# Kernel tuning notes

Measured on AMD Instinct MI355X. Metric: run time of the kernel, lower is better.

Reference implementation:

```python
import jax, jax.numpy as jnp
import numpy as np

HEADS = 8  # from init_kwargs

def setup_inputs() -> dict:
    key = jax.random.key(0)
    ks = jax.random.split(key, 9)
    N, S, E = 8, 2048, 512
    scale = 1.0 / np.sqrt(E)
    return {
        "values": jax.random.normal(ks[0], (N, S, E), jnp.float32),
        "keys": jax.random.normal(ks[1], (N, S, E), jnp.float32),
        "query": jax.random.normal(ks[2], (N, S, E), jnp.float32),
        "mask": jnp.ones((N, 1, 1, S), jnp.int32),
        "Wv": jax.random.normal(ks[3], (E, E), jnp.float32) * scale,
        "Wk": jax.random.normal(ks[4], (E, E), jnp.float32) * scale,
        "Wq": jax.random.normal(ks[5], (E, E), jnp.float32) * scale,
        "Wo": jax.random.normal(ks[6], (E, E), jnp.float32) * scale,
        "bo": jnp.zeros((E,), jnp.float32),
    }

def reference(values, keys, query, mask, Wv, Wk, Wq, Wo, bo):
    N, Q, E = query.shape
    H = HEADS
    D = E // H
    v = (values @ Wv).reshape(N, -1, H, D)  # [N,K,H,D]
    k = (keys @ Wk).reshape(N, -1, H, D)
    q = (query @ Wq).reshape(N, Q, H, D)
    energy = jnp.einsum('nqhd,nkhd->nhqk', q, k)  # [N,H,Q,K]
    energy = jnp.where(mask == 0, jnp.float32(-1e20), energy)
    attn = jax.nn.softmax(energy / jnp.sqrt(jnp.float32(D)), axis=3)
    out = jnp.einsum('nhqk,nkhd->nqhd', attn, v).reshape(N, Q, E)
    return out @ Wo + bo
```

## Files before the change

kernel.cpp:

```cpp
#include <hip/hip_runtime.h>
#include <hip/hip_bf16.h>
#include <stdint.h>

typedef __bf16 bf16;
typedef __bf16 bf16x8 __attribute__((ext_vector_type(8)));
typedef __bf16 bf16x4v __attribute__((ext_vector_type(4)));
typedef float  f32x4  __attribute__((ext_vector_type(4)));
typedef float  f32x16 __attribute__((ext_vector_type(16)));
typedef unsigned int u32x4 __attribute__((ext_vector_type(4)));

#define NB    8
#define SEQ   2048
#define EMB   512
#define NHEAD 8
#define HD    64

static __device__ __forceinline__ f32x4 mfma16(bf16x8 a, bf16x8 b, f32x4 c) {
    return __builtin_amdgcn_mfma_f32_16x16x32_bf16(a, b, c, 0, 0, 0);
}
static __device__ __forceinline__ f32x16 mfma32(bf16x8 a, bf16x8 b, f32x16 c) {
    return __builtin_amdgcn_mfma_f32_32x32x16_bf16(a, b, c, 0, 0, 0);
}
static __device__ __forceinline__ float ex2(float x) {
    float r; asm("v_exp_f32 %0, %1" : "=v"(r) : "v"(x)); return r;
}
static __device__ __forceinline__ unsigned pkbf(float lo, float hi) {
    unsigned d; asm("v_cvt_pk_bf16_f32 %0, %1, %2" : "=v"(d) : "v"(lo), "v"(hi)); return d;
}
static __device__ __forceinline__ void gload_lds16(const void* g, void* l) {
    __builtin_amdgcn_global_load_lds(
        (const __attribute__((address_space(1))) unsigned int*)g,
        (__attribute__((address_space(3))) unsigned int*)l, 16, 0, 0);
}
static __device__ __forceinline__ int vposInv(int pos) {
    int p4  = pos >> 4;
    int r   = ((p4 & 1) << 3) | (pos & 7);
    int hi2 = (pos >> 3) & 1;
    return (p4 >> 1) * 32 + ((r & 3) | (hi2 << 2) | ((r >> 2) << 3));
}
#define PRIO1 __builtin_amdgcn_s_setprio(1)
#define PRIO0 __builtin_amdgcn_s_setprio(0)

__global__ __launch_bounds__(256) void prep_weights(
    const float* __restrict__ Wv, const float* __restrict__ Wk,
    const float* __restrict__ Wq, const float* __restrict__ Wo,
    bf16* __restrict__ wt)
{
    __shared__ float Ls[64][65];
    const int b    = blockIdx.x;
    const int wsel = b >> 6;
    const int kt   = (b & 63) >> 3;
    const int nt   = b & 7;
    const int t    = threadIdx.x;
    const float* src = (wsel == 0) ? Wv : (wsel == 1) ? Wk : (wsel == 2) ? Wq : Wo;

#pragma unroll
    for (int i = 0; i < 16; ++i) {
        int e = i * 256 + t;
        int k = e >> 6, n = e & 63;
        Ls[k][n] = src[(size_t)(kt * 64 + k) * 512 + nt * 64 + n];
    }
    __syncthreads();
#pragma unroll
    for (int i = 0; i < 16; ++i) {
        int e = i * 256 + t;
        int n = e >> 6, k = e & 63;
        wt[(size_t)wsel * 262144 + (size_t)(nt * 64 + n) * 512 + kt * 64 + k] = (bf16)Ls[k][n];
    }
}

__global__ __launch_bounds__(256) void proj_fused(
    const float* __restrict__ Av, const float* __restrict__ Ak,
    const float* __restrict__ Aq, const bf16* __restrict__ wt,
    bf16* __restrict__ VbP, bf16* __restrict__ Kb, bf16* __restrict__ Qb,
    float sc)
{
    __shared__ __align__(16) char smem[35328];
    bf16* As = (bf16*)smem;
    char* BsB = smem + 18432;

    const int t    = threadIdx.x;
    const int lane = t & 63;
    const int wave = t >> 6;
    const int wr   = wave >> 1, wc = wave & 1;
    const int l15  = lane & 15, lg = lane >> 4;
    const int z    = blockIdx.z;
    const long row0 = (long)blockIdx.x * 128;
    const int  col0 = blockIdx.y * 128;

    const float* A  = (z == 0) ? Av : (z == 1) ? Ak : Aq;
    const bf16*  Bt = wt + (size_t)z * 262144;
    const float  oscale = (z == 2) ? sc : 1.0f;

    f32x4 acc[4][4];
#pragma unroll
    for (int i = 0; i < 4; i++)
#pragma unroll
        for (int j = 0; j < 4; j++) acc[i][j] = (f32x4){0.f, 0.f, 0.f, 0.f};

    for (int k0 = 0; k0 < 512; k0 += 64) {
        __syncthreads();
#pragma unroll
        for (int i = 0; i < 8; i++) {
            int c  = t + 256 * i;
            int r  = c >> 4;
            int cc = (c & 15) * 4;
            f32x4 v = *(const f32x4*)(A + (row0 + r) * 512 + k0 + cc);
            bf16x4v pk = { (bf16)v[0], (bf16)v[1], (bf16)v[2], (bf16)v[3] };
            *(bf16x4v*)(As + r * 72 + cc) = pk;
        }
#pragma unroll
        for (int i = 0; i < 4; i++) {
            int chunk = i * 4 + wave;
            int c = chunk * 64 + lane;
            int r = c >> 3, u = c & 7;
            gload_lds16(Bt + (size_t)(col0 + r) * 512 + k0 + ((u ^ (r & 7)) << 3),
                        BsB + chunk * 1024);
        }
        __syncthreads();
#pragma unroll
        for (int kc = 0; kc < 64; kc += 32) {
            bf16x8 af[4], bfv[4];
#pragma unroll
            for (int mb = 0; mb < 4; mb++)
                af[mb] = *(bf16x8*)(As + (wr * 64 + mb * 16 + l15) * 72 + kc + lg * 8);
#pragma unroll
            for (int nb = 0; nb < 4; nb++) {
                int row = wc * 64 + nb * 16 + l15;
                bfv[nb] = *(bf16x8*)(BsB + row * 128 + (((lg + (kc >> 3)) ^ (l15 & 7)) << 4));
            }
#pragma unroll
            for (int mb = 0; mb < 4; mb++)
#pragma unroll
                for (int nb = 0; nb < 4; nb++)
                    acc[mb][nb] = mfma16(af[mb], bfv[nb], acc[mb][nb]);
        }
    }

    if (z == 0) {
        __syncthreads();
        bf16* Cs = (bf16*)smem;
#pragma unroll
        for (int mb = 0; mb < 4; mb++)
#pragma unroll
            for (int nb = 0; nb < 4; nb++)
#pragma unroll
                for (int r = 0; r < 4; r++) {
                    int keyl = wr * 64 + mb * 16 + lg * 4 + r;
                    int dl   = wc * 64 + nb * 16 + l15;
                    Cs[dl * 138 + keyl] = (bf16)acc[mb][nb][r];
                }
        __syncthreads();
        const int n_idx = (int)(row0 >> 11);
        const int key0  = (int)(row0 & 2047);
        const int dl    = t >> 1;
        const int half  = t & 1;
        const int x8    = (dl & 7) << 3;
        bf16* dst = VbP + ((size_t)n_idx * 512 + col0 + dl) * 2048 + key0 + half * 64;
#pragma unroll
        for (int cc = 0; cc < 8; ++cc) {
            bf16x8 v;
#pragma unroll
            for (int j = 0; j < 8; ++j)
                v[j] = Cs[dl * 138 + half * 64 + vposInv((cc * 8 + j) ^ x8)];
            *(bf16x8*)(dst + cc * 8) = v;
        }
    } else {
        bf16* Cp = (z == 1) ? Kb : Qb;
#pragma unroll
        for (int mb = 0; mb < 4; mb++)
#pragma unroll
            for (int nb = 0; nb < 4; nb++)
#pragma unroll
                for (int r = 0; r < 4; r++) {
                    long grow = row0 + wr * 64 + mb * 16 + lg * 4 + r;
                    int  gcol = col0 + wc * 64 + nb * 16 + l15;
                    Cp[grow * 512 + gcol] = (bf16)(acc[mb][nb][r] * oscale);
                }
    }
}

__global__ __launch_bounds__(256) void gemm_final(
    const bf16* __restrict__ Ap, const bf16* __restrict__ Bt,
    float* __restrict__ Cp, const float* __restrict__ bias)
{
    __shared__ __align__(16) char AsM[128 * 128];
    __shared__ __align__(16) bf16 Bs[128][64];

    const int t    = threadIdx.x;
    const int lane = t & 63;
    const int wave = t >> 6;
    const int wr   = wave >> 1, wc = wave & 1;
    const int l15  = lane & 15, lg = lane >> 4;
    const long row0 = (long)blockIdx.x * 128;
    const int  col0 = blockIdx.y * 128;

    f32x4 acc[4][4];
#pragma unroll
    for (int i = 0; i < 4; i++)
#pragma unroll
        for (int j = 0; j < 4; j++) acc[i][j] = (f32x4){0.f, 0.f, 0.f, 0.f};

    for (int k0 = 0; k0 < 512; k0 += 64) {
        __syncthreads();
#pragma unroll
        for (int i = 0; i < 4; i++) {
            int chunk = i * 4 + wave;
            int c = chunk * 64 + lane;
            int r = c >> 3, u = c & 7;
            gload_lds16(Ap + (row0 + r) * 512 + k0 + ((u ^ (r & 7)) << 3),
                        AsM + chunk * 1024);
        }
#pragma unroll
        for (int i = 0; i < 4; i++) {
            int chunk = i * 4 + wave;
            int c = chunk * 64 + lane;
            int r = c >> 3, u = c & 7;
            gload_lds16(Bt + (size_t)(col0 + r) * 512 + k0 + ((u ^ (r & 7)) << 3),
                        (char*)&Bs[0][0] + chunk * 1024);
        }
        __syncthreads();
#pragma unroll
        for (int kc = 0; kc < 64; kc += 32) {
            bf16x8 af[4], bfv[4];
#pragma unroll
            for (int mb = 0; mb < 4; mb++) {
                int row = wr * 64 + mb * 16 + l15;
                af[mb] = *(bf16x8*)(AsM + row * 128 + (((lg + (kc >> 3)) ^ (l15 & 7)) << 4));
            }
#pragma unroll
            for (int nb = 0; nb < 4; nb++) {
                int row = wc * 64 + nb * 16 + l15;
                bfv[nb] = *(bf16x8*)((char*)&Bs[0][0] + row * 128 + (((lg + (kc >> 3)) ^ (l15 & 7)) << 4));
            }
#pragma unroll
            for (int mb = 0; mb < 4; mb++)
#pragma unroll
                for (int nb = 0; nb < 4; nb++)
                    acc[mb][nb] = mfma16(af[mb], bfv[nb], acc[mb][nb]);
        }
    }

#pragma unroll
    for (int mb = 0; mb < 4; mb++)
#pragma unroll
        for (int nb = 0; nb < 4; nb++)
#pragma unroll
            for (int r = 0; r < 4; r++) {
                long grow = row0 + wr * 64 + mb * 16 + lg * 4 + r;
                int  gcol = col0 + wc * 64 + nb * 16 + l15;
                Cp[grow * 512 + gcol] = acc[mb][nb][r] + bias[gcol];
            }
}

__global__ __launch_bounds__(512, 2) void attn_kernel(
    const bf16* __restrict__ Qg, const bf16* __restrict__ Kg,
    const bf16* __restrict__ VbP, const int* __restrict__ mask,
    bf16* __restrict__ ctx)
{
    __shared__ __align__(16) char smem[65536];

    const int t    = threadIdx.x;
    const int lane = t & 63;
    const int w    = t >> 6;
    const int l31  = lane & 31;
    const int hi   = lane >> 5;
    const int h = blockIdx.x, n = blockIdx.y, qt = blockIdx.z;

    const size_t nbase   = (size_t)n * SEQ;
    const size_t headoff = (size_t)h * 64;
    const int q0 = qt * 256 + w * 32;

    {
        const int* mp0 = mask + n * SEQ + t * 4;
        int mok = (mp0[0] != 0) & (mp0[1] != 0) & (mp0[2] != 0) & (mp0[3] != 0);
        unsigned long long b = __ballot(mok);
        if (lane == 0) ((int*)smem)[w] = (b == ~0ULL) ? 1 : 0;
    }
    __syncthreads();
    int maskall = 1;
#pragma unroll
    for (int i = 0; i < 8; ++i) maskall &= ((int*)smem)[i];
    __syncthreads();

    bf16x8 qf[4];
#pragma unroll
    for (int ds = 0; ds < 4; ++ds)
        qf[ds] = *(const bf16x8*)(Qg + (nbase + q0 + l31) * 512 + headoff + ds * 16 + hi * 8);

    f32x16 o[2] = {};
    float l_run = 0.f;

    const bf16* kg = Kg + (nbase + w * 8 + (lane >> 3)) * 512 + headoff + (((lane & 7) ^ (lane >> 3)) << 3);
    const bf16* vgP = VbP + ((size_t)n * 512 + h * 64 + w * 8 + (lane >> 3)) * 2048 + ((lane & 7) << 3);
    const int*  mp = mask + n * SEQ;

    gload_lds16(kg,                    smem + 0 * 8192 + w * 1024);
    gload_lds16(kg + (size_t)64 * 512, smem + 1 * 8192 + w * 1024);
    gload_lds16(vgP,                   smem + 32768 + 0 * 8192 + w * 1024);
    gload_lds16(vgP + 64,              smem + 32768 + 1 * 8192 + w * 1024);
    __syncthreads();

    f32x16 p[2];
    u32x4  bq[4];

#define QK_TILE(BUF) do {                                                     \
        const char* kbb = smem + (BUF) * 8192;                                \
        f32x16 zz = {};                                                       \
        p[0] = zz; p[1] = zz;                                                 \
        PRIO1;                                                                \
        _Pragma("unroll")                                                     \
        for (int ds = 0; ds < 4; ++ds) {                                      \
            int sw = (ds * 32 + hi * 16) ^ ((l31 & 7) << 4);                  \
            bf16x8 kf0 = *(const bf16x8*)(kbb + l31 * 128 + sw);              \
            bf16x8 kf1 = *(const bf16x8*)(kbb + (32 + l31) * 128 + sw);       \
            p[0] = mfma32(kf0, qf[ds], p[0]);                                 \
            p[1] = mfma32(kf1, qf[ds], p[1]);                                 \
        }                                                                     \
        PRIO0;                                                                \
    } while (0)

#define MASK_TILE(T) do {                                                     \
        if (!maskall) {                                                       \
            int mv = mp[(T) * 64 + lane];                                     \
            unsigned long long mb = __ballot(mv != 0);                        \
            if (mb != ~0ULL) {                                                \
                _Pragma("unroll") for (int kb = 0; kb < 2; ++kb) {            \
                    float* pp = (float*)&p[kb];                               \
                    _Pragma("unroll") for (int r = 0; r < 16; ++r) {          \
                        int kk = kb * 32 + (r & 3) + 8 * (r >> 2) + 4 * hi;   \
                        if (!((mb >> kk) & 1)) pp[r] = -1e30f;                \
                    }                                                         \
                }                                                             \
            }                                                                 \
        }                                                                     \
    } while (0)

#define SM_PACK do {                                                          \
        float* p0 = (float*)&p[0];                                            \
        float* p1 = (float*)&p[1];                                            \
        float sa0 = 0.f, sa1 = 0.f, sa2 = 0.f, sa3 = 0.f;                     \
        _Pragma("unroll") for (int r = 0; r < 16; r += 4) {                   \
            float e0 = ex2(p0[r]);   p0[r]   = e0; sa0 += e0;                 \
            float e1 = ex2(p0[r+1]); p0[r+1] = e1; sa1 += e1;                 \
            float e2 = ex2(p0[r+2]); p0[r+2] = e2; sa2 += e2;                 \
            float e3 = ex2(p0[r+3]); p0[r+3] = e3; sa3 += e3;                 \
        }                                                                     \
        _Pragma("unroll") for (int r = 0; r < 16; r += 4) {                   \
            float e0 = ex2(p1[r]);   p1[r]   = e0; sa0 += e0;                 \
            float e1 = ex2(p1[r+1]); p1[r+1] = e1; sa1 += e1;                 \
            float e2 = ex2(p1[r+2]); p1[r+2] = e2; sa2 += e2;                 \
            float e3 = ex2(p1[r+3]); p1[r+3] = e3; sa3 += e3;                 \
        }                                                                     \
        float sl = (sa0 + sa1) + (sa2 + sa3);                                 \
        l_run += sl + __shfl_xor(sl, 32);                                     \
        _Pragma("unroll")                                                     \
        for (int ks = 0; ks < 4; ++ks) {                                      \
            float* ps = (ks >> 1) ? p1 : p0;                                  \
            int bo = (ks & 1) * 8;                                            \
            bq[ks] = (u32x4){ pkbf(ps[bo + 0], ps[bo + 1]),                   \
                              pkbf(ps[bo + 2], ps[bo + 3]),                   \
                              pkbf(ps[bo + 4], ps[bo + 5]),                   \
                              pkbf(ps[bo + 6], ps[bo + 7]) };                 \
        }                                                                     \
    } while (0)

#define PV_TILE(BUF) do {                                                     \
        const char* vbb = smem + 32768 + (BUF) * 8192;                        \
        PRIO1;                                                                \
        _Pragma("unroll")                                                     \
        for (int ks = 0; ks < 4; ++ks) {                                      \
            int sw = (ks * 32 + hi * 16) ^ ((l31 & 7) << 4);                  \
            bf16x8 vf0 = *(const bf16x8*)(vbb + l31 * 128 + sw);              \
            bf16x8 vf1 = *(const bf16x8*)(vbb + (32 + l31) * 128 + sw);       \
            union { u32x4 u; bf16x8 v; } c0;                                  \
            c0.u = bq[ks];                                                    \
            o[0] = mfma32(vf0, c0.v, o[0]);                                   \
            o[1] = mfma32(vf1, c0.v, o[1]);                                   \
        }                                                                     \
        PRIO0;                                                                \
    } while (0)

    for (int e = 0; e < 16; ++e) {
        const int bA = (e & 1) * 2, bB = bA + 1;
        const int nA = bA ^ 2,      nB = bB ^ 2;
        if (e < 15) {
            gload_lds16(kg + (size_t)(2 * e + 2) * 64 * 512, smem + nA * 8192 + w * 1024);
            gload_lds16(kg + (size_t)(2 * e + 3) * 64 * 512, smem + nB * 8192 + w * 1024);
            gload_lds16(vgP + (2 * e + 2) * 64, smem + 32768 + nA * 8192 + w * 1024);
            gload_lds16(vgP + (2 * e + 3) * 64, smem + 32768 + nB * 8192 + w * 1024);
        }
        QK_TILE(bA);
        MASK_TILE(2 * e);
        SM_PACK;
        PV_TILE(bA);
        QK_TILE(bB);
        MASK_TILE(2 * e + 1);
        SM_PACK;
        PV_TILE(bB);
        __syncthreads();
    }

    {
        float inv = 1.f / l_run;
        bf16* ob = (bf16*)(smem + w * 4608);
#pragma unroll
        for (int db = 0; db < 2; ++db) {
            float* oo = (float*)&o[db];
#pragma unroll
            for (int r = 0; r < 16; ++r) {
                int d = db * 32 + (r & 3) + 8 * (r >> 2) + 4 * hi;
                ob[l31 * 72 + d] = (bf16)(oo[r] * inv);
            }
        }
        __syncthreads();
#pragma unroll
        for (int i = 0; i < 2; ++i)
#pragma unroll
            for (int half = 0; half < 2; ++half) {
                int ql = i * 16 + (lane >> 2);
                int d8 = (lane & 3) * 8 + half * 32;
                bf16x8 vv = *(const bf16x8*)(ob + ql * 72 + d8);
                *(bf16x8*)(ctx + (nbase + q0 + ql) * 512 + headoff + d8) = vv;
            }
    }
#undef QK_TILE
#undef MASK_TILE
#undef SM_PACK
#undef PV_TILE
}

extern "C" void kernel_launch(void* const* d_in, const int* in_sizes, int n_in,
                              void* d_out, int out_size, void* d_ws, size_t ws_size,
                              hipStream_t stream) {
    (void)in_sizes; (void)n_in; (void)out_size; (void)ws_size;
    const float* values = (const float*)d_in[0];
    const float* keys   = (const float*)d_in[1];
    const float* query  = (const float*)d_in[2];
    const int*   mask   = (const int*)d_in[3];
    const float* Wv = (const float*)d_in[4];
    const float* Wk = (const float*)d_in[5];
    const float* Wq = (const float*)d_in[6];
    const float* Wo = (const float*)d_in[7];
    const float* bo = (const float*)d_in[8];
    float* out = (float*)d_out;

    char* ws = (char*)d_ws;
    bf16* wt  = (bf16*)(ws);
    bf16* Qb  = (bf16*)(ws + ((size_t)2  << 20));
    bf16* Kb  = (bf16*)(ws + ((size_t)18 << 20));
    bf16* VbP = (bf16*)(ws + ((size_t)34 << 20));
    bf16* Cb  = (bf16*)(ws + ((size_t)50 << 20));

    const float SC = 0.18033688011f;

    prep_weights<<<256, 256, 0, stream>>>(Wv, Wk, Wq, Wo, wt);
    proj_fused<<<dim3(128, 4, 3), 256, 0, stream>>>(values, keys, query, wt,
                                                    VbP, Kb, Qb, SC);
    attn_kernel<<<dim3(8, 8, 8), 512, 0, stream>>>(Qb, Kb, VbP, mask, Cb);
    gemm_final<<<dim3(128, 4), 256, 0, stream>>>(Cb, wt + 3 * 262144, out, bo);
}
```

Measured before the change: 154.2 us.

## Double-buffer LDS tiles in projection and output GEMMs to overlap loads

Both the fused QKV projection GEMM and the final output GEMM now use two LDS buffers per operand. The next K-slice is prefetched while MFMAs run on the current one, and one barrier per iteration replaces two. The aim is to hide global-load latency behind compute. In exchange, LDS use roughly doubles (about 68 KB and 64 KB per block), which can lower occupancy. In the projection kernel, the fp32 A-tile is loaded into registers and converted synchronously, so that path still stalls on its loads.

```diff
diff --git a/kernel.cpp b/kernel.cpp
--- a/kernel.cpp
+++ b/kernel.cpp
@@ -75,9 +75,7 @@
     bf16* __restrict__ VbP, bf16* __restrict__ Kb, bf16* __restrict__ Qb,
     float sc)
 {
-    __shared__ __align__(16) char smem[35328];
-    bf16* As = (bf16*)smem;
-    char* BsB = smem + 18432;
+    __shared__ __align__(16) char smem[69632];
 
     const int t    = threadIdx.x;
     const int lane = t & 63;
@@ -98,36 +96,49 @@
 #pragma unroll
         for (int j = 0; j < 4; j++) acc[i][j] = (f32x4){0.f, 0.f, 0.f, 0.f};
 
-    for (int k0 = 0; k0 < 512; k0 += 64) {
-        __syncthreads();
-#pragma unroll
-        for (int i = 0; i < 8; i++) {
-            int c  = t + 256 * i;
-            int r  = c >> 4;
-            int cc = (c & 15) * 4;
-            f32x4 v = *(const f32x4*)(A + (row0 + r) * 512 + k0 + cc);
-            bf16x4v pk = { (bf16)v[0], (bf16)v[1], (bf16)v[2], (bf16)v[3] };
-            *(bf16x4v*)(As + r * 72 + cc) = pk;
-        }
-#pragma unroll
-        for (int i = 0; i < 4; i++) {
-            int chunk = i * 4 + wave;
-            int c = chunk * 64 + lane;
-            int r = c >> 3, u = c & 7;
-            gload_lds16(Bt + (size_t)(col0 + r) * 512 + k0 + ((u ^ (r & 7)) << 3),
-                        BsB + chunk * 1024);
-        }
-        __syncthreads();
+#define STAGE_A(K0, BUF) do {                                                 \
+        _Pragma("unroll") for (int i = 0; i < 8; i++) {                       \
+            int c  = t + 256 * i;                                             \
+            int r  = c >> 4;                                                  \
+            int cc = (c & 15) * 4;                                            \
+            f32x4 v = *(const f32x4*)(A + (row0 + r) * 512 + (K0) + cc);      \
+            bf16x4v pk = { (bf16)v[0], (bf16)v[1], (bf16)v[2], (bf16)v[3] };  \
+            *(bf16x4v*)(smem + (BUF) * 18432 + r * 144 + cc * 2) = pk;        \
+        }                                                                     \
+    } while (0)
+
+#define STAGE_B(K0, BUF) do {                                                 \
+        _Pragma("unroll") for (int i = 0; i < 4; i++) {                       \
+            int chunk = i * 4 + wave;                                         \
+            int c = chunk * 64 + lane;                                        \
+            int r = c >> 3, u = c & 7;                                        \
+            gload_lds16(Bt + (size_t)(col0 + r) * 512 + (K0) + ((u ^ (r & 7)) << 3), \
+                        smem + 36864 + (BUF) * 16384 + chunk * 1024);         \
+        }                                                                     \
+    } while (0)
+
+    STAGE_B(0, 0);
+    STAGE_A(0, 0);
+
+    for (int ks = 0; ks < 8; ++ks) {
+        const int cur = ks & 1;
+        __syncthreads();
+        if (ks < 7) {
+            STAGE_B(64 * (ks + 1), cur ^ 1);
+            STAGE_A(64 * (ks + 1), cur ^ 1);
+        }
 #pragma unroll
         for (int kc = 0; kc < 64; kc += 32) {
             bf16x8 af[4], bfv[4];
 #pragma unroll
             for (int mb = 0; mb < 4; mb++)
-                af[mb] = *(bf16x8*)(As + (wr * 64 + mb * 16 + l15) * 72 + kc + lg * 8);
+                af[mb] = *(bf16x8*)(smem + cur * 18432 +
+                                    (wr * 64 + mb * 16 + l15) * 144 + (kc + lg * 8) * 2);
 #pragma unroll
             for (int nb = 0; nb < 4; nb++) {
                 int row = wc * 64 + nb * 16 + l15;
-                bfv[nb] = *(bf16x8*)(BsB + row * 128 + (((lg + (kc >> 3)) ^ (l15 & 7)) << 4));
+                bfv[nb] = *(bf16x8*)(smem + 36864 + cur * 16384 +
+                                     row * 128 + (((lg + (kc >> 3)) ^ (l15 & 7)) << 4));
             }
 #pragma unroll
             for (int mb = 0; mb < 4; mb++)
@@ -136,6 +147,8 @@
                     acc[mb][nb] = mfma16(af[mb], bfv[nb], acc[mb][nb]);
         }
     }
+#undef STAGE_A
+#undef STAGE_B
 
     if (z == 0) {
         __syncthreads();
@@ -184,8 +197,7 @@
     const bf16* __restrict__ Ap, const bf16* __restrict__ Bt,
     float* __restrict__ Cp, const float* __restrict__ bias)
 {
-    __shared__ __align__(16) char AsM[128 * 128];
-    __shared__ __align__(16) bf16 Bs[128][64];
+    __shared__ __align__(16) char smem[65536];
 
     const int t    = threadIdx.x;
     const int lane = t & 63;
@@ -201,37 +213,38 @@
 #pragma unroll
         for (int j = 0; j < 4; j++) acc[i][j] = (f32x4){0.f, 0.f, 0.f, 0.f};
 
-    for (int k0 = 0; k0 < 512; k0 += 64) {
-        __syncthreads();
-#pragma unroll
-        for (int i = 0; i < 4; i++) {
-            int chunk = i * 4 + wave;
-            int c = chunk * 64 + lane;
-            int r = c >> 3, u = c & 7;
-            gload_lds16(Ap + (row0 + r) * 512 + k0 + ((u ^ (r & 7)) << 3),
-                        AsM + chunk * 1024);
-        }
-#pragma unroll
-        for (int i = 0; i < 4; i++) {
-            int chunk = i * 4 + wave;
-            int c = chunk * 64 + lane;
-            int r = c >> 3, u = c & 7;
-            gload_lds16(Bt + (size_t)(col0 + r) * 512 + k0 + ((u ^ (r & 7)) << 3),
-                        (char*)&Bs[0][0] + chunk * 1024);
-        }
-        __syncthreads();
+#define STAGE_AB(K0, BUF) do {                                                \
+        _Pragma("unroll") for (int i = 0; i < 4; i++) {                       \
+            int chunk = i * 4 + wave;                                         \
+            int c = chunk * 64 + lane;                                        \
+            int r = c >> 3, u = c & 7;                                        \
+            gload_lds16(Ap + (row0 + r) * 512 + (K0) + ((u ^ (r & 7)) << 3),  \
+                        smem + (BUF) * 16384 + chunk * 1024);                 \
+            gload_lds16(Bt + (size_t)(col0 + r) * 512 + (K0) + ((u ^ (r & 7)) << 3), \
+                        smem + 32768 + (BUF) * 16384 + chunk * 1024);         \
+        }                                                                     \
+    } while (0)
+
+    STAGE_AB(0, 0);
+
+    for (int ks = 0; ks < 8; ++ks) {
+        const int cur = ks & 1;
+        __syncthreads();
+        if (ks < 7) STAGE_AB(64 * (ks + 1), cur ^ 1);
 #pragma unroll
         for (int kc = 0; kc < 64; kc += 32) {
             bf16x8 af[4], bfv[4];
 #pragma unroll
             for (int mb = 0; mb < 4; mb++) {
                 int row = wr * 64 + mb * 16 + l15;
-                af[mb] = *(bf16x8*)(AsM + row * 128 + (((lg + (kc >> 3)) ^ (l15 & 7)) << 4));
+                af[mb] = *(bf16x8*)(smem + cur * 16384 +
+                                    row * 128 + (((lg + (kc >> 3)) ^ (l15 & 7)) << 4));
             }
 #pragma unroll
             for (int nb = 0; nb < 4; nb++) {
                 int row = wc * 64 + nb * 16 + l15;
-                bfv[nb] = *(bf16x8*)((char*)&Bs[0][0] + row * 128 + (((lg + (kc >> 3)) ^ (l15 & 7)) << 4));
+                bfv[nb] = *(bf16x8*)(smem + 32768 + cur * 16384 +
+                                     row * 128 + (((lg + (kc >> 3)) ^ (l15 & 7)) << 4));
             }
 #pragma unroll
             for (int mb = 0; mb < 4; mb++)
@@ -240,6 +253,7 @@
                     acc[mb][nb] = mfma16(af[mb], bfv[nb], acc[mb][nb]);
         }
     }
+#undef STAGE_AB
 
 #pragma unroll
     for (int mb = 0; mb < 4; mb++)
```

After: 151.0 us, median of 2. -2.0%, faster.
